# Kernel optimization log

Measured on AMD Instinct MI355X. Metric: run time of the kernel, lower is better.

## Reference

```python
import jax, jax.numpy as jnp
import numpy as np
import math

ROPE_THETA = 10000.0


def apply_rope(x, positions):
    # x: [B, H, S, d_k], positions: [S]
    d_k = x.shape[-1]
    inv_freq = 1.0 / (ROPE_THETA ** (jnp.arange(0, d_k, 2, dtype=jnp.float32) / d_k))  # [d_k/2]
    angles = positions.astype(jnp.float32)[:, None] * inv_freq[None, :]  # [S, d_k/2]
    cos = jnp.cos(angles)
    sin = jnp.sin(angles)
    x1 = x[..., 0::2]
    x2 = x[..., 1::2]
    r1 = x1 * cos - x2 * sin
    r2 = x1 * sin + x2 * cos
    out = jnp.stack([r1, r2], axis=-1)  # interleave pairs back
    return out.reshape(x.shape)


def setup_inputs() -> dict:
    key = jax.random.key(0)
    k1, k2, k3 = jax.random.split(key, 3)
    B, S, D = 4, 2048, 1024
    x = jax.random.normal(k1, (B, S, D), dtype=jnp.float32)
    token_positions = jnp.arange(S, dtype=jnp.int32)
    w_qkv = jax.random.normal(k2, (3 * D, D), dtype=jnp.float32) * (1.0 / math.sqrt(D))
    w_o = jax.random.normal(k3, (D, D), dtype=jnp.float32) * (1.0 / math.sqrt(D))
    return {"x": x, "token_positions": token_positions, "w_qkv": w_qkv, "w_o": w_o}


def reference(x, token_positions, w_qkv, w_o):
    B, S, D = x.shape
    H = 16
    d_k = D // H
    qkv = jnp.einsum('bsd,ed->bse', x, w_qkv)  # [B, S, 3D]
    # rearrange '... s (stack h dk) -> stack ... h s dk'
    qkv = qkv.reshape(B, S, 3, H, d_k)
    q = jnp.transpose(qkv[:, :, 0], (0, 2, 1, 3))  # [B, H, S, dk]
    k = jnp.transpose(qkv[:, :, 1], (0, 2, 1, 3))
    v = jnp.transpose(qkv[:, :, 2], (0, 2, 1, 3))
    q = apply_rope(q, token_positions)
    k = apply_rope(k, token_positions)
    scores = jnp.einsum('bhqd,bhkd->bhqk', q, k) / math.sqrt(d_k)
    causal = jnp.tril(jnp.ones((S, S), dtype=bool))
    scores = jnp.where(causal[None, None], scores, -jnp.inf)
    attn = jax.nn.softmax(scores, axis=-1)
    out = jnp.einsum('bhqk,bhkd->bhqd', attn, v)  # [B, H, S, dk]
    out = jnp.transpose(out, (0, 2, 1, 3)).reshape(B, S, D)
    return jnp.einsum('bsd,ed->bse', out, w_o)
```

## Files before the change

### kernel.cpp

```cpp
#include <hip/hip_runtime.h>
#include <hip/hip_bf16.h>
#include <math.h>

typedef __bf16 bf16_t;
typedef __attribute__((ext_vector_type(8))) __bf16 bf16x8;
typedef __attribute__((ext_vector_type(4))) __bf16 bf16x4;
typedef __attribute__((ext_vector_type(4))) float f32x4;

#define MFMA_16x16x32(A_, B_, C_) __builtin_amdgcn_mfma_f32_16x16x32_bf16((A_), (B_), (C_), 0, 0, 0)

#define Bsz 4
#define Ssz 2048
#define Dsz 1024
#define Hh 16
#define DKd 64
#define Mrows (Bsz * Ssz)
#define N1 (3 * Dsz)
#define KD Dsz

__global__ void cvt_f32_bf16_kernel(const float* __restrict__ src, bf16_t* __restrict__ dst, int n4) {
  int i = blockIdx.x * blockDim.x + threadIdx.x;
  if (i >= n4) return;
  float4 v = reinterpret_cast<const float4*>(src)[i];
  bf16x4 o = {(bf16_t)v.x, (bf16_t)v.y, (bf16_t)v.z, (bf16_t)v.w};
  reinterpret_cast<bf16x4*>(dst)[i] = o;
}

__global__ void rope_tab_kernel(const int* __restrict__ pos, float2* __restrict__ tab) {
  int i = blockIdx.x * blockDim.x + threadIdx.x;
  if (i >= Ssz * 32) return;
  int s = i >> 5, f = i & 31;
  float inv_freq = powf(10000.0f, -(float)(2 * f) / 64.0f);
  float a = (float)pos[s] * inv_freq;
  tab[i] = make_float2(cosf(a), sinf(a));
}

__global__ __launch_bounds__(512, 2) void gemm256_qkv_kernel(
    const bf16_t* __restrict__ A, const bf16_t* __restrict__ Bt,
    bf16_t* __restrict__ qb, bf16_t* __restrict__ kb, bf16_t* __restrict__ vtb,
    const float2* __restrict__ tab) {
  __shared__ __align__(16) bf16_t As[2][256 * 64];
  __shared__ __align__(16) bf16_t Bs[2][256 * 64];
  const int t = threadIdx.x;
  const int w = t >> 6, l = t & 63;
  const int lr = l & 15, lk = l >> 4;
  const int rs = lr >> 1;
  const int wm = w >> 2, wn = w & 3;
  const int m0 = blockIdx.y * 256, n0 = blockIdx.x * 256;

  const int trow = t >> 3;
  const int schunk = (t & 7) ^ ((t >> 4) & 7);
  const bf16_t* gAs[4];
  const bf16_t* gBs[4];
#pragma unroll
  for (int i = 0; i < 4; ++i) {
    gAs[i] = A + (size_t)(m0 + i * 64 + trow) * KD + schunk * 8;
    gBs[i] = Bt + (size_t)(n0 + i * 64 + trow) * KD + schunk * 8;
  }

  f32x4 acc[8][4] = {};

#pragma unroll
  for (int i = 0; i < 4; ++i) {
    __builtin_amdgcn_global_load_lds(gAs[i], &As[0][(i * 64 + w * 8) * 64], 16, 0, 0);
    __builtin_amdgcn_global_load_lds(gBs[i], &Bs[0][(i * 64 + w * 8) * 64], 16, 0, 0);
  }
  __syncthreads();

  for (int tt = 0; tt < KD / 64; ++tt) {
    const int b = tt & 1;
    if (tt + 1 < KD / 64) {
      const int kt = (tt + 1) * 64;
#pragma unroll
      for (int i = 0; i < 4; ++i) {
        __builtin_amdgcn_global_load_lds(gAs[i] + kt, &As[b ^ 1][(i * 64 + w * 8) * 64], 16, 0, 0);
        __builtin_amdgcn_global_load_lds(gBs[i] + kt, &Bs[b ^ 1][(i * 64 + w * 8) * 64], 16, 0, 0);
      }
    }
    bf16x8 bfv[4][2];
#pragma unroll
    for (int n = 0; n < 4; ++n) {
      const int R = wn * 64 + n * 16 + lr;
#pragma unroll
      for (int ks = 0; ks < 2; ++ks)
        bfv[n][ks] = *reinterpret_cast<const bf16x8*>(&Bs[b][R * 64 + (((ks * 4 + lk) ^ rs) * 8)]);
    }
#pragma unroll
    for (int mp = 0; mp < 4; ++mp) {
      bf16x8 af[2][2];
#pragma unroll
      for (int mi = 0; mi < 2; ++mi) {
        const int R = wm * 128 + (mp * 2 + mi) * 16 + lr;
#pragma unroll
        for (int ks = 0; ks < 2; ++ks)
          af[mi][ks] = *reinterpret_cast<const bf16x8*>(&As[b][R * 64 + (((ks * 4 + lk) ^ rs) * 8)]);
      }
      __builtin_amdgcn_s_setprio(1);
#pragma unroll
      for (int mi = 0; mi < 2; ++mi)
#pragma unroll
        for (int n = 0; n < 4; ++n) {
          acc[mp * 2 + mi][n] = MFMA_16x16x32(af[mi][0], bfv[n][0], acc[mp * 2 + mi][n]);
          acc[mp * 2 + mi][n] = MFMA_16x16x32(af[mi][1], bfv[n][1], acc[mp * 2 + mi][n]);
        }
      __builtin_amdgcn_s_setprio(0);
    }
    __syncthreads();
  }

  const int sect = n0 >> 10;
  const int hh = ((n0 + wn * 64) >> 6) & 15;
  if (sect < 2) {
#pragma unroll
    for (int m = 0; m < 8; ++m)
#pragma unroll
      for (int r = 0; r < 4; ++r) {
        const int grow = m0 + wm * 128 + m * 16 + lk * 4 + r;
        const int bb = grow >> 11, s = grow & (Ssz - 1);
        const float2* tr = tab + (s << 5);
        bf16_t* basep = (sect == 0 ? qb : kb) + ((size_t)(bb * Hh + hh) * Ssz + s) * DKd;
#pragma unroll
        for (int n = 0; n < 4; ++n) {
          const float v = acc[m][n][r];
          const float pv = __shfl_xor(v, 1);
          const int dk = n * 16 + lr;
          const float2 cs = tr[dk >> 1];
          float vr = (dk & 1) ? (pv * cs.y + v * cs.x) : (v * cs.x - pv * cs.y);
          if (sect == 0) vr *= 0.125f;
          basep[dk] = (bf16_t)vr;
        }
      }
  } else {
#pragma unroll
    for (int m = 0; m < 8; ++m)
#pragma unroll
      for (int r = 0; r < 4; ++r) {
        const int grow = m0 + wm * 128 + m * 16 + lk * 4 + r;
        const int bb = grow >> 11, s = grow & (Ssz - 1);
        bf16_t* vb = vtb + (size_t)(bb * Hh + hh) * DKd * Ssz + s;
#pragma unroll
        for (int n = 0; n < 4; ++n)
          vb[(size_t)(n * 16 + lr) * Ssz] = (bf16_t)acc[m][n][r];
      }
  }
}

__global__ __launch_bounds__(256, 3) void gemm_out_kernel(
    const bf16_t* __restrict__ A, const bf16_t* __restrict__ Bt, int Kdim, int ldcN,
    float* __restrict__ fout) {
  __shared__ __align__(16) bf16_t As[2][128 * 32];
  __shared__ __align__(16) bf16_t Bs[2][128 * 32];
  const int t = threadIdx.x;
  const int w = t >> 6, l = t & 63;
  const int lr = l & 15, lk = l >> 4;
  const int wm = w >> 1, wn = w & 1;
  const int m0 = blockIdx.y * 128, n0 = blockIdx.x * 128;

  const int srow = t >> 2;
  const int schunk = (t & 3) ^ ((t >> 3) & 3);
  const bf16_t* gA = A + (size_t)(m0 + srow) * Kdim + schunk * 8;
  const bf16_t* gB = Bt + (size_t)(n0 + srow) * Kdim + schunk * 8;

  f32x4 acc[4][4] = {};
  const int rsw = (lr >> 1) & 3;

#define STAGE_(PH, KT)                                                                   \
  do {                                                                                   \
    __builtin_amdgcn_global_load_lds(gA + (KT), &As[PH][(w * 16) * 32], 16, 0, 0);       \
    __builtin_amdgcn_global_load_lds(gA + (size_t)64 * Kdim + (KT),                      \
                                     &As[PH][(64 + w * 16) * 32], 16, 0, 0);             \
    __builtin_amdgcn_global_load_lds(gB + (KT), &Bs[PH][(w * 16) * 32], 16, 0, 0);       \
    __builtin_amdgcn_global_load_lds(gB + (size_t)64 * Kdim + (KT),                      \
                                     &Bs[PH][(64 + w * 16) * 32], 16, 0, 0);             \
  } while (0)

#define COMPUTE_(PH)                                                                     \
  do {                                                                                   \
    bf16x8 af[4], bfv[4];                                                                \
    _Pragma("unroll") for (int m = 0; m < 4; ++m) af[m] =                                \
        *reinterpret_cast<const bf16x8*>(&As[PH][(wm * 64 + m * 16 + lr) * 32] +         \
                                         ((lk ^ rsw) * 8));                              \
    _Pragma("unroll") for (int n = 0; n < 4; ++n) bfv[n] =                               \
        *reinterpret_cast<const bf16x8*>(&Bs[PH][(wn * 64 + n * 16 + lr) * 32] +         \
                                         ((lk ^ rsw) * 8));                              \
    _Pragma("unroll") for (int m = 0; m < 4; ++m) _Pragma("unroll") for (int n = 0;      \
                                                                         n < 4; ++n)    \
        acc[m][n] = MFMA_16x16x32(af[m], bfv[n], acc[m][n]);                             \
  } while (0)

  STAGE_(0, 0);
  __syncthreads();
  for (int kt = 0; kt < Kdim; kt += 64) {
    STAGE_(1, kt + 32);
    COMPUTE_(0);
    __syncthreads();
    if (kt + 64 < Kdim) STAGE_(0, kt + 64);
    COMPUTE_(1);
    __syncthreads();
  }
#undef STAGE_
#undef COMPUTE_

#pragma unroll
  for (int m = 0; m < 4; ++m)
#pragma unroll
    for (int r = 0; r < 4; ++r) {
      const int grow = m0 + wm * 64 + m * 16 + lk * 4 + r;
      float* op = fout + (size_t)grow * ldcN + n0 + wn * 64 + lr;
#pragma unroll
      for (int n = 0; n < 4; ++n) op[n * 16] = acc[m][n][r];
    }
}

__global__ __launch_bounds__(256, 3) void attn_kernel(
    const bf16_t* __restrict__ qb, const bf16_t* __restrict__ kb,
    const bf16_t* __restrict__ vtb, bf16_t* __restrict__ aout) {
  __shared__ __align__(16) bf16_t Ks[64 * 64];
  __shared__ __align__(16) bf16_t Vs[64 * 64];
  const int t = threadIdx.x, w = t >> 6, l = t & 63;
  const int lr = l & 15, lk = l >> 4;
  const int bid = blockIdx.x;
  const int bh = (bid & 7) * 8 + ((bid >> 3) & 7);
  const int qt = 15 - (bid >> 6);
  const int q0 = qt * 128;
  const int sub0 = q0 + w * 32;

  const bf16_t* qbase = qb + ((size_t)bh * Ssz + sub0) * DKd;
  bf16x8 qf[2][2];
#pragma unroll
  for (int s = 0; s < 2; ++s) {
    qf[s][0] = *reinterpret_cast<const bf16x8*>(qbase + (s * 16 + lr) * DKd + lk * 8);
    qf[s][1] = *reinterpret_cast<const bf16x8*>(qbase + (s * 16 + lr) * DKd + 32 + lk * 8);
  }

  f32x4 o[2][4] = {};
  float mrow[2] = {-INFINITY, -INFINITY};
  float lsum[2] = {0.f, 0.f};

  const int srow = t >> 2;
  const int scc = (t & 3) * 2;
  const bf16_t* kg = kb + ((size_t)bh * Ssz + srow) * DKd + scc * 8;
  const bf16_t* vg = vtb + ((size_t)bh * DKd + srow) * Ssz + scc * 8;
  bf16_t* ksw0 = Ks + srow * 64 + ((scc ^ (srow & 7)) * 8);
  bf16_t* ksw1 = Ks + srow * 64 + (((scc + 1) ^ (srow & 7)) * 8);
  bf16_t* vw[4];
#pragma unroll
  for (int u = 0; u < 2; ++u) {
    const int c = scc + u;
    const int B = 32 * (c >> 2) + 16 * (c & 1) + 4 * ((c & 3) >> 1);
    const int ch = B >> 3, off = B & 7;
    vw[2 * u] = Vs + srow * 64 + ((ch ^ (srow & 7)) * 8) + off;
    vw[2 * u + 1] = Vs + srow * 64 + (((ch + 1) ^ (srow & 7)) * 8) + off;
  }

  const int kvend = q0 + 128;
  bf16x8 pk0 = *reinterpret_cast<const bf16x8*>(kg);
  bf16x8 pk1 = *reinterpret_cast<const bf16x8*>(kg + 8);
  bf16x8 pv0 = *reinterpret_cast<const bf16x8*>(vg);
  bf16x8 pv1 = *reinterpret_cast<const bf16x8*>(vg + 8);

  for (int kv = 0; kv < kvend; kv += 64) {
    __syncthreads();
    *reinterpret_cast<bf16x8*>(ksw0) = pk0;
    *reinterpret_cast<bf16x8*>(ksw1) = pk1;
    *reinterpret_cast<bf16x4*>(vw[0]) = __builtin_shufflevector(pv0, pv0, 0, 1, 2, 3);
    *reinterpret_cast<bf16x4*>(vw[1]) = __builtin_shufflevector(pv0, pv0, 4, 5, 6, 7);
    *reinterpret_cast<bf16x4*>(vw[2]) = __builtin_shufflevector(pv1, pv1, 0, 1, 2, 3);
    *reinterpret_cast<bf16x4*>(vw[3]) = __builtin_shufflevector(pv1, pv1, 4, 5, 6, 7);
    __syncthreads();
    if (kv + 64 < kvend) {
      pk0 = *reinterpret_cast<const bf16x8*>(kg + (size_t)(kv + 64) * DKd);
      pk1 = *reinterpret_cast<const bf16x8*>(kg + (size_t)(kv + 64) * DKd + 8);
      pv0 = *reinterpret_cast<const bf16x8*>(vg + kv + 64);
      pv1 = *reinterpret_cast<const bf16x8*>(vg + kv + 64 + 8);
    }
#pragma unroll
    for (int s = 0; s < 2; ++s) {
      const int subrow = sub0 + s * 16;
      if (kv > subrow + 15) continue;
      f32x4 sa[4];
#pragma unroll
      for (int n = 0; n < 4; ++n) {
        const int R = n * 16 + lr;
        const bf16x8 a0 = *reinterpret_cast<const bf16x8*>(Ks + R * 64 + ((lk ^ (R & 7)) * 8));
        const bf16x8 a1 = *reinterpret_cast<const bf16x8*>(Ks + R * 64 + (((lk + 4) ^ (R & 7)) * 8));
        f32x4 z = {};
        z = MFMA_16x16x32(a0, qf[s][0], z);
        z = MFMA_16x16x32(a1, qf[s][1], z);
        sa[n] = z;
      }
      if (kv + 63 > subrow) {
        const int qrow = subrow + lr;
        const int kbase = kv + lk * 4;
#pragma unroll
        for (int n = 0; n < 4; ++n)
#pragma unroll
          for (int r = 0; r < 4; ++r)
            if (kbase + n * 16 + r > qrow) sa[n][r] = -INFINITY;
      }
      float mx = fmaxf(fmaxf(fmaxf(sa[0][0], sa[0][1]), fmaxf(sa[0][2], sa[0][3])),
                       fmaxf(fmaxf(sa[1][0], sa[1][1]), fmaxf(sa[1][2], sa[1][3])));
      mx = fmaxf(mx, fmaxf(fmaxf(fmaxf(sa[2][0], sa[2][1]), fmaxf(sa[2][2], sa[2][3])),
                           fmaxf(fmaxf(sa[3][0], sa[3][1]), fmaxf(sa[3][2], sa[3][3]))));
      mx = fmaxf(mx, __shfl_xor(mx, 16));
      mx = fmaxf(mx, __shfl_xor(mx, 32));
      const float mnew = fmaxf(mrow[s], mx);
      const float scl = __expf(mrow[s] - mnew);
      mrow[s] = mnew;
      float ps = 0.f;
#pragma unroll
      for (int n = 0; n < 4; ++n)
#pragma unroll
        for (int r = 0; r < 4; ++r) {
          const float p = __expf(sa[n][r] - mnew);
          sa[n][r] = p;
          ps += p;
        }
      lsum[s] = lsum[s] * scl + ps;
#pragma unroll
      for (int n = 0; n < 4; ++n)
#pragma unroll
        for (int r = 0; r < 4; ++r) o[s][n][r] *= scl;
      bf16x8 pb0, pb1;
#pragma unroll
      for (int r = 0; r < 4; ++r) {
        pb0[r] = (bf16_t)sa[0][r];
        pb0[4 + r] = (bf16_t)sa[1][r];
        pb1[r] = (bf16_t)sa[2][r];
        pb1[4 + r] = (bf16_t)sa[3][r];
      }
#pragma unroll
      for (int n = 0; n < 4; ++n) {
        const int R = n * 16 + lr;
        const bf16x8 v0 = *reinterpret_cast<const bf16x8*>(Vs + R * 64 + ((lk ^ (R & 7)) * 8));
        const bf16x8 v1 = *reinterpret_cast<const bf16x8*>(Vs + R * 64 + (((lk + 4) ^ (R & 7)) * 8));
        o[s][n] = MFMA_16x16x32(v0, pb0, o[s][n]);
        o[s][n] = MFMA_16x16x32(v1, pb1, o[s][n]);
      }
    }
  }
  const int b_ = bh >> 4, h_ = bh & 15;
#pragma unroll
  for (int s = 0; s < 2; ++s) {
    float sm = lsum[s];
    sm += __shfl_xor(sm, 16);
    sm += __shfl_xor(sm, 32);
    const float inv = 1.0f / sm;
    const int qrow = sub0 + s * 16 + lr;
    bf16_t* op = aout + ((size_t)b_ * Ssz + qrow) * Dsz + h_ * DKd + lk * 4;
#pragma unroll
    for (int n = 0; n < 4; ++n) {
      const bf16x4 ov = {(bf16_t)(o[s][n][0] * inv), (bf16_t)(o[s][n][1] * inv),
                         (bf16_t)(o[s][n][2] * inv), (bf16_t)(o[s][n][3] * inv)};
      *reinterpret_cast<bf16x4*>(op + n * 16) = ov;
    }
  }
}

extern "C" void kernel_launch(void* const* d_in, const int* in_sizes, int n_in,
                              void* d_out, int out_size, void* d_ws, size_t ws_size,
                              hipStream_t stream) {
  const float* x = (const float*)d_in[0];
  const int* pos = (const int*)d_in[1];
  const float* wqkv = (const float*)d_in[2];
  const float* wo = (const float*)d_in[3];
  float* out = (float*)d_out;

  bf16_t* xb = (bf16_t*)d_ws;
  bf16_t* wqkvb = xb + (size_t)Mrows * KD;
  bf16_t* wob = wqkvb + (size_t)N1 * KD;
  bf16_t* qbuf = wob + (size_t)Dsz * KD;
  bf16_t* kbuf = qbuf + (size_t)64 * Ssz * DKd;
  bf16_t* vtb = kbuf + (size_t)64 * Ssz * DKd;
  float2* tab = (float2*)(vtb + (size_t)64 * Ssz * DKd);
  bf16_t* aout = xb;

  {
    int n4 = Mrows * KD / 4;
    cvt_f32_bf16_kernel<<<(n4 + 255) / 256, 256, 0, stream>>>(x, xb, n4);
  }
  {
    int n4 = N1 * KD / 4;
    cvt_f32_bf16_kernel<<<(n4 + 255) / 256, 256, 0, stream>>>(wqkv, wqkvb, n4);
  }
  {
    int n4 = Dsz * KD / 4;
    cvt_f32_bf16_kernel<<<(n4 + 255) / 256, 256, 0, stream>>>(wo, wob, n4);
  }
  rope_tab_kernel<<<(Ssz * 32 + 255) / 256, 256, 0, stream>>>(pos, tab);

  gemm256_qkv_kernel<<<dim3(N1 / 256, Mrows / 256), 512, 0, stream>>>(
      xb, wqkvb, qbuf, kbuf, vtb, tab);

  attn_kernel<<<dim3(16 * 64), 256, 0, stream>>>(qbuf, kbuf, vtb, aout);

  gemm_out_kernel<<<dim3(Dsz / 128, Mrows / 128), 256, 0, stream>>>(
      aout, wob, KD, Dsz, out);
}
```

Before: 197.9 us.

## Deepen QKV GEMM pipeline to four-stage K=32 ring with manual vmcnt waits

The QKV projection GEMM moves from a double-buffered K=64 loop to a four-buffer ring of K=32 slices, keeping three global-to-LDS prefetches in flight. It uses explicit s_waitcnt vmcnt counts and one barrier per step instead of __syncthreads, and precomputes swizzled LDS read offsets. Launch bounds drop to one block per CU, trading occupancy for deeper latency hiding of global loads. The manual wait counts depend on exactly four loads per thread per stage being issued.

```diff
diff --git a/kernel.cpp b/kernel.cpp
--- a/kernel.cpp
+++ b/kernel.cpp
@@ -35,78 +35,78 @@
   tab[i] = make_float2(cosf(a), sinf(a));
 }
 
-__global__ __launch_bounds__(512, 2) void gemm256_qkv_kernel(
+__global__ __launch_bounds__(512, 1) void gemm256_qkv_kernel(
     const bf16_t* __restrict__ A, const bf16_t* __restrict__ Bt,
     bf16_t* __restrict__ qb, bf16_t* __restrict__ kb, bf16_t* __restrict__ vtb,
     const float2* __restrict__ tab) {
-  __shared__ __align__(16) bf16_t As[2][256 * 64];
-  __shared__ __align__(16) bf16_t Bs[2][256 * 64];
+  constexpr int NSTEPS = KD / 32;
+  __shared__ __align__(16) bf16_t As[4][256 * 32];
+  __shared__ __align__(16) bf16_t Bs[4][256 * 32];
   const int t = threadIdx.x;
   const int w = t >> 6, l = t & 63;
   const int lr = l & 15, lk = l >> 4;
-  const int rs = lr >> 1;
   const int wm = w >> 2, wn = w & 3;
   const int m0 = blockIdx.y * 256, n0 = blockIdx.x * 256;
 
-  const int trow = t >> 3;
-  const int schunk = (t & 7) ^ ((t >> 4) & 7);
-  const bf16_t* gAs[4];
-  const bf16_t* gBs[4];
-#pragma unroll
-  for (int i = 0; i < 4; ++i) {
-    gAs[i] = A + (size_t)(m0 + i * 64 + trow) * KD + schunk * 8;
-    gBs[i] = Bt + (size_t)(n0 + i * 64 + trow) * KD + schunk * 8;
-  }
+  const int gcol = ((t & 3) ^ ((t >> 3) & 3)) * 8;
+  const bf16_t* gA0 = A + (size_t)(m0 + (t >> 2)) * KD + gcol;
+  const bf16_t* gA1 = gA0 + (size_t)128 * KD;
+  const bf16_t* gB0 = Bt + (size_t)(n0 + (t >> 2)) * KD + gcol;
+  const bf16_t* gB1 = gB0 + (size_t)128 * KD;
+  const int ldsoff0 = w * 512;
+  const int ldsoff1 = 4096 + w * 512;
+
+  int aOffE[8], bOffE[4];
+  const int rxor = (lr >> 1) & 3;
+#pragma unroll
+  for (int m = 0; m < 8; ++m)
+    aOffE[m] = (wm * 128 + m * 16 + lr) * 32 + ((lk ^ rxor) * 8);
+#pragma unroll
+  for (int n = 0; n < 4; ++n)
+    bOffE[n] = (wn * 64 + n * 16 + lr) * 32 + ((lk ^ rxor) * 8);
 
   f32x4 acc[8][4] = {};
 
 #pragma unroll
-  for (int i = 0; i < 4; ++i) {
-    __builtin_amdgcn_global_load_lds(gAs[i], &As[0][(i * 64 + w * 8) * 64], 16, 0, 0);
-    __builtin_amdgcn_global_load_lds(gBs[i], &Bs[0][(i * 64 + w * 8) * 64], 16, 0, 0);
-  }
-  __syncthreads();
-
-  for (int tt = 0; tt < KD / 64; ++tt) {
-    const int b = tt & 1;
-    if (tt + 1 < KD / 64) {
-      const int kt = (tt + 1) * 64;
-#pragma unroll
-      for (int i = 0; i < 4; ++i) {
-        __builtin_amdgcn_global_load_lds(gAs[i] + kt, &As[b ^ 1][(i * 64 + w * 8) * 64], 16, 0, 0);
-        __builtin_amdgcn_global_load_lds(gBs[i] + kt, &Bs[b ^ 1][(i * 64 + w * 8) * 64], 16, 0, 0);
-      }
-    }
-    bf16x8 bfv[4][2];
-#pragma unroll
-    for (int n = 0; n < 4; ++n) {
-      const int R = wn * 64 + n * 16 + lr;
-#pragma unroll
-      for (int ks = 0; ks < 2; ++ks)
-        bfv[n][ks] = *reinterpret_cast<const bf16x8*>(&Bs[b][R * 64 + (((ks * 4 + lk) ^ rs) * 8)]);
-    }
-#pragma unroll
-    for (int mp = 0; mp < 4; ++mp) {
-      bf16x8 af[2][2];
-#pragma unroll
-      for (int mi = 0; mi < 2; ++mi) {
-        const int R = wm * 128 + (mp * 2 + mi) * 16 + lr;
-#pragma unroll
-        for (int ks = 0; ks < 2; ++ks)
-          af[mi][ks] = *reinterpret_cast<const bf16x8*>(&As[b][R * 64 + (((ks * 4 + lk) ^ rs) * 8)]);
-      }
-      __builtin_amdgcn_s_setprio(1);
-#pragma unroll
-      for (int mi = 0; mi < 2; ++mi)
-#pragma unroll
-        for (int n = 0; n < 4; ++n) {
-          acc[mp * 2 + mi][n] = MFMA_16x16x32(af[mi][0], bfv[n][0], acc[mp * 2 + mi][n]);
-          acc[mp * 2 + mi][n] = MFMA_16x16x32(af[mi][1], bfv[n][1], acc[mp * 2 + mi][n]);
-        }
-      __builtin_amdgcn_s_setprio(0);
-    }
-    __syncthreads();
-  }
+  for (int i = 0; i < 3; ++i) {
+    __builtin_amdgcn_global_load_lds(gA0 + i * 32, &As[i][ldsoff0], 16, 0, 0);
+    __builtin_amdgcn_global_load_lds(gA1 + i * 32, &As[i][ldsoff1], 16, 0, 0);
+    __builtin_amdgcn_global_load_lds(gB0 + i * 32, &Bs[i][ldsoff0], 16, 0, 0);
+    __builtin_amdgcn_global_load_lds(gB1 + i * 32, &Bs[i][ldsoff1], 16, 0, 0);
+  }
+
+#define K_STEP_BODY(S_, VMSTR_)                                                      \
+  do {                                                                               \
+    asm volatile(VMSTR_ ::: "memory");                                               \
+    __builtin_amdgcn_s_barrier();                                                    \
+    __builtin_amdgcn_sched_barrier(0);                                               \
+    if ((S_) + 3 < NSTEPS) {                                                         \
+      const int rb_ = ((S_) + 3) & 3;                                                \
+      const int kt_ = ((S_) + 3) * 32;                                               \
+      __builtin_amdgcn_global_load_lds(gA0 + kt_, &As[rb_][ldsoff0], 16, 0, 0);      \
+      __builtin_amdgcn_global_load_lds(gA1 + kt_, &As[rb_][ldsoff1], 16, 0, 0);      \
+      __builtin_amdgcn_global_load_lds(gB0 + kt_, &Bs[rb_][ldsoff0], 16, 0, 0);      \
+      __builtin_amdgcn_global_load_lds(gB1 + kt_, &Bs[rb_][ldsoff1], 16, 0, 0);      \
+    }                                                                                \
+    const bf16_t* Ab_ = As[(S_) & 3];                                                \
+    const bf16_t* Bb_ = Bs[(S_) & 3];                                                \
+    bf16x8 af_[8], bf_[4];                                                           \
+    _Pragma("unroll") for (int n_ = 0; n_ < 4; ++n_) bf_[n_] =                       \
+        *reinterpret_cast<const bf16x8*>(Bb_ + bOffE[n_]);                           \
+    _Pragma("unroll") for (int m_ = 0; m_ < 8; ++m_) af_[m_] =                       \
+        *reinterpret_cast<const bf16x8*>(Ab_ + aOffE[m_]);                           \
+    __builtin_amdgcn_s_setprio(1);                                                   \
+    _Pragma("unroll") for (int m_ = 0; m_ < 8; ++m_)                                 \
+      _Pragma("unroll") for (int n_ = 0; n_ < 4; ++n_)                               \
+          acc[m_][n_] = MFMA_16x16x32(af_[m_], bf_[n_], acc[m_][n_]);                \
+    __builtin_amdgcn_s_setprio(0);                                                   \
+  } while (0)
+
+#pragma unroll 1
+  for (int s = 0; s < NSTEPS - 2; ++s) K_STEP_BODY(s, "s_waitcnt vmcnt(8)");
+  K_STEP_BODY(NSTEPS - 2, "s_waitcnt vmcnt(4)");
+  K_STEP_BODY(NSTEPS - 1, "s_waitcnt vmcnt(0)");
+#undef K_STEP_BODY
 
   const int sect = n0 >> 10;
   const int hh = ((n0 + wn * 64) >> 6) & 15;
```

New measurement: 208.5 us. 1.05x slower.
